# Optimization experiments

Hardware: AMD Instinct MI355X
Metric: run time of the kernel (lower is better)

## Reference

```python
import jax, jax.numpy as jnp
import numpy as np

def setup_inputs() -> dict:
    key = jax.random.key(0)
    ks = jax.random.split(key, 6)
    B, H, Dk, Dv = 128, 16, 128, 128
    return {
        "q": jax.random.normal(ks[0], (B, H, 1, Dk), dtype=jnp.float32),
        "k": jax.random.normal(ks[1], (B, H, 1, Dk), dtype=jnp.float32),
        "v": jax.random.normal(ks[2], (B, H, 1, Dv), dtype=jnp.float32),
        "g": jax.random.uniform(ks[3], (B, H, 1), dtype=jnp.float32),
        "beta": jax.random.uniform(ks[4], (B, H, 1), dtype=jnp.float32),
        "last_recurrent_state": jax.random.normal(ks[5], (B, H, Dk, Dv), dtype=jnp.float32),
    }

def reference(q, k, v, g, beta, last_recurrent_state):
    # q,k: (B,H,1,Dk); v: (B,H,1,Dv); g,beta: (B,H,1); state: (B,H,Dk,Dv)
    q_t = q[:, :, 0, :]                      # (B,H,Dk)
    k_t = k[:, :, 0, :]                      # (B,H,Dk)
    v_t = v[:, :, 0, :]                      # (B,H,Dv)
    decay = jnp.exp(g)[..., None]            # (B,H,1,1)
    state = last_recurrent_state * decay     # (B,H,Dk,Dv)
    kv_mem = jnp.einsum('bhkv,bhk->bhv', state, k_t)   # (B,H,Dv)
    delta = (v_t - kv_mem) * beta            # (B,H,Dv)
    state = state + k_t[..., :, None] * delta[..., None, :]  # outer update
    out = jnp.einsum('bhkv,bhk->bhv', state, q_t)       # (B,H,Dv)
    out = out[:, :, None, :]                 # (B,H,1,Dv)
    return jnp.concatenate([out.reshape(-1), state.reshape(-1)], axis=0)
```

## Files before the change

### kernel.cpp

```cpp
#include <hip/hip_runtime.h>


#define DK 128
#define DV 128
#define VS 32
typedef float f4 __attribute__((ext_vector_type(4)));

__global__ __launch_bounds__(256) void s1_cell_kernel(
    const float* __restrict__ q,
    const float* __restrict__ k,
    const float* __restrict__ v,
    const float* __restrict__ g,
    const float* __restrict__ beta,
    const float* __restrict__ S,
    float* __restrict__ out,
    int BH)
{
    const int bh    = blockIdx.x >> 2;
    const int sl    = blockIdx.x & 3;
    const int vbase = sl * VS;

    const size_t stile = (size_t)bh * DK * DV;
    const float* __restrict__ Sb   = S + stile + vbase;
    float* __restrict__ out_o      = out + (size_t)bh * DV + vbase;
    float* __restrict__ out_S      = out + (size_t)BH * DV + stile + vbase;

    __shared__ float kt[DK];
    __shared__ float qt[DK];
    __shared__ float vt[VS];
    __shared__ float apart[32][VS];
    __shared__ float bpart[32][VS];
    __shared__ float sdelta[VS];
    __shared__ float s_kq;

    const int t = threadIdx.x;

    if (t < DK) {
        kt[t] = k[bh * DK + t];
        qt[t] = q[bh * DK + t];
    }
    if (t < VS) vt[t] = v[bh * DV + vbase + t];
    __syncthreads();

    const float decay = expf(g[bh]);
    const float bta   = beta[bh];

    if (t < 64) {
        float val = kt[t] * qt[t] + kt[t + 64] * qt[t + 64];
        #pragma unroll
        for (int off = 32; off > 0; off >>= 1)
            val += __shfl_down(val, off, 64);
        if (t == 0) s_kq = val;
    }

    const int vc = (t & 7) * 4;
    const int rb = t >> 3;

    f4 s[4];
    float a0 = 0.f, a1 = 0.f, a2 = 0.f, a3 = 0.f;
    float b0 = 0.f, b1 = 0.f, b2 = 0.f, b3 = 0.f;

    #pragma unroll
    for (int i = 0; i < 4; ++i) {
        const int r = rb + 32 * i;
        s[i] = *(const f4*)(Sb + (size_t)r * DV + vc);
        const float kv = kt[r];
        const float qv = qt[r];
        a0 += s[i].x * kv;  a1 += s[i].y * kv;  a2 += s[i].z * kv;  a3 += s[i].w * kv;
        b0 += s[i].x * qv;  b1 += s[i].y * qv;  b2 += s[i].z * qv;  b3 += s[i].w * qv;
    }
    *(f4*)&apart[rb][vc] = (f4){a0, a1, a2, a3};
    *(f4*)&bpart[rb][vc] = (f4){b0, b1, b2, b3};
    __syncthreads();

    if (t < VS) {
        float A = 0.f, Bq = 0.f;
        #pragma unroll
        for (int j = 0; j < 32; ++j) {
            A  += apart[j][t];
            Bq += bpart[j][t];
        }
        const float dlt = (vt[t] - decay * A) * bta;
        sdelta[t] = dlt;
        __builtin_nontemporal_store(decay * Bq + s_kq * dlt, &out_o[t]);
    }
    __syncthreads();

    const f4 d = *(const f4*)&sdelta[vc];

    #pragma unroll
    for (int i = 0; i < 4; ++i) {
        const int r = rb + 32 * i;
        const float ktk = kt[r];
        f4 w;
        w.x = decay * s[i].x + ktk * d.x;
        w.y = decay * s[i].y + ktk * d.y;
        w.z = decay * s[i].z + ktk * d.z;
        w.w = decay * s[i].w + ktk * d.w;
        __builtin_nontemporal_store(w, (f4*)(out_S + (size_t)r * DV + vc));
    }
}

extern "C" void kernel_launch(void* const* d_in, const int* in_sizes, int n_in,
                              void* d_out, int out_size, void* d_ws, size_t ws_size,
                              hipStream_t stream) {
    const float* q    = (const float*)d_in[0];
    const float* k    = (const float*)d_in[1];
    const float* v    = (const float*)d_in[2];
    const float* g    = (const float*)d_in[3];
    const float* beta = (const float*)d_in[4];
    const float* S    = (const float*)d_in[5];
    float* out = (float*)d_out;

    const int BH = in_sizes[3];

    s1_cell_kernel<<<BH * 4, 256, 0, stream>>>(q, k, v, g, beta, S, out, BH);
}
```

Measured before the change: 248.7 us.

## Map each 128x32 state slice to one wavefront with shuffle reductions

Each wavefront now owns one (bh, column-slice) task, with each lane holding a 16x4 patch of the state in registers. Shared-memory staging, cross-thread partial sums and all block barriers are replaced by xor-shuffle reductions across the row groups, and k/q/v are loaded straight from global memory. This removes synchronization and LDS traffic on a memory-bound kernel. In exchange each lane keeps 16 float4 values live, which raises register pressure, and the grid has four times fewer blocks.

```diff
diff --git a/kernel.cpp b/kernel.cpp
--- a/kernel.cpp
+++ b/kernel.cpp
@@ -6,7 +6,7 @@
 #define VS 32
 typedef float f4 __attribute__((ext_vector_type(4)));
 
-__global__ __launch_bounds__(256) void s1_cell_kernel(
+__global__ __launch_bounds__(256, 4) void s1_cell_kernel(
     const float* __restrict__ q,
     const float* __restrict__ k,
     const float* __restrict__ v,
@@ -16,88 +16,74 @@
     float* __restrict__ out,
     int BH)
 {
-    const int bh    = blockIdx.x >> 2;
-    const int sl    = blockIdx.x & 3;
-    const int vbase = sl * VS;
+    const int wid  = threadIdx.x >> 6;
+    const int lane = threadIdx.x & 63;
+    const int task = (blockIdx.x << 2) + wid;
+    const int bh   = task >> 2;
+    const int sl   = task & 3;
+
+    const int vgrp = lane & 7;
+    const int kgrp = lane >> 3;
+    const int colf = sl * VS + vgrp * 4;
+    const int row0 = kgrp * 16;
 
     const size_t stile = (size_t)bh * DK * DV;
-    const float* __restrict__ Sb   = S + stile + vbase;
-    float* __restrict__ out_o      = out + (size_t)bh * DV + vbase;
-    float* __restrict__ out_S      = out + (size_t)BH * DV + stile + vbase;
-
-    __shared__ float kt[DK];
-    __shared__ float qt[DK];
-    __shared__ float vt[VS];
-    __shared__ float apart[32][VS];
-    __shared__ float bpart[32][VS];
-    __shared__ float sdelta[VS];
-    __shared__ float s_kq;
-
-    const int t = threadIdx.x;
-
-    if (t < DK) {
-        kt[t] = k[bh * DK + t];
-        qt[t] = q[bh * DK + t];
-    }
-    if (t < VS) vt[t] = v[bh * DV + vbase + t];
-    __syncthreads();
+    const float* __restrict__ Sp = S   + stile + (size_t)row0 * DV + colf;
+    float* __restrict__ So = out + (size_t)BH * DV + stile + (size_t)row0 * DV + colf;
 
     const float decay = expf(g[bh]);
     const float bta   = beta[bh];
 
-    if (t < 64) {
-        float val = kt[t] * qt[t] + kt[t + 64] * qt[t + 64];
-        #pragma unroll
-        for (int off = 32; off > 0; off >>= 1)
-            val += __shfl_down(val, off, 64);
-        if (t == 0) s_kq = val;
+    f4 kt[4];
+    #pragma unroll
+    for (int j = 0; j < 4; ++j)
+        kt[j] = *(const f4*)(k + bh * DK + row0 + 4 * j);
+
+    const f4 vv = *(const f4*)(v + bh * DV + colf);
+
+    f4 s[16];
+    #pragma unroll
+    for (int i = 0; i < 16; ++i)
+        s[i] = *(const f4*)(Sp + (size_t)i * DV);
+
+    f4 a = {0.f, 0.f, 0.f, 0.f};
+    f4 b = {0.f, 0.f, 0.f, 0.f};
+    float kq = 0.f;
+    #pragma unroll
+    for (int j = 0; j < 4; ++j) {
+        const f4 qj = *(const f4*)(q + bh * DK + row0 + 4 * j);
+        const f4 kj = kt[j];
+        a += s[4*j+0] * kj.x;  b += s[4*j+0] * qj.x;
+        a += s[4*j+1] * kj.y;  b += s[4*j+1] * qj.y;
+        a += s[4*j+2] * kj.z;  b += s[4*j+2] * qj.z;
+        a += s[4*j+3] * kj.w;  b += s[4*j+3] * qj.w;
+        kq += kj.x*qj.x + kj.y*qj.y + kj.z*qj.z + kj.w*qj.w;
     }
 
-    const int vc = (t & 7) * 4;
-    const int rb = t >> 3;
+    #pragma unroll
+    for (int m = 8; m <= 32; m <<= 1) {
+        a.x += __shfl_xor(a.x, m, 64);
+        a.y += __shfl_xor(a.y, m, 64);
+        a.z += __shfl_xor(a.z, m, 64);
+        a.w += __shfl_xor(a.w, m, 64);
+        b.x += __shfl_xor(b.x, m, 64);
+        b.y += __shfl_xor(b.y, m, 64);
+        b.z += __shfl_xor(b.z, m, 64);
+        b.w += __shfl_xor(b.w, m, 64);
+        kq  += __shfl_xor(kq,  m, 64);
+    }
 
-    f4 s[4];
-    float a0 = 0.f, a1 = 0.f, a2 = 0.f, a3 = 0.f;
-    float b0 = 0.f, b1 = 0.f, b2 = 0.f, b3 = 0.f;
+    const f4 dlt = (vv - decay * a) * bta;
+    if (kgrp == 0) {
+        const f4 o = decay * b + kq * dlt;
+        __builtin_nontemporal_store(o, (f4*)(out + (size_t)bh * DV + colf));
+    }
 
     #pragma unroll
-    for (int i = 0; i < 4; ++i) {
-        const int r = rb + 32 * i;
-        s[i] = *(const f4*)(Sb + (size_t)r * DV + vc);
-        const float kv = kt[r];
-        const float qv = qt[r];
-        a0 += s[i].x * kv;  a1 += s[i].y * kv;  a2 += s[i].z * kv;  a3 += s[i].w * kv;
-        b0 += s[i].x * qv;  b1 += s[i].y * qv;  b2 += s[i].z * qv;  b3 += s[i].w * qv;
-    }
-    *(f4*)&apart[rb][vc] = (f4){a0, a1, a2, a3};
-    *(f4*)&bpart[rb][vc] = (f4){b0, b1, b2, b3};
-    __syncthreads();
-
-    if (t < VS) {
-        float A = 0.f, Bq = 0.f;
-        #pragma unroll
-        for (int j = 0; j < 32; ++j) {
-            A  += apart[j][t];
-            Bq += bpart[j][t];
-        }
-        const float dlt = (vt[t] - decay * A) * bta;
-        sdelta[t] = dlt;
-        __builtin_nontemporal_store(decay * Bq + s_kq * dlt, &out_o[t]);
-    }
-    __syncthreads();
-
-    const f4 d = *(const f4*)&sdelta[vc];
-
-    #pragma unroll
-    for (int i = 0; i < 4; ++i) {
-        const int r = rb + 32 * i;
-        const float ktk = kt[r];
-        f4 w;
-        w.x = decay * s[i].x + ktk * d.x;
-        w.y = decay * s[i].y + ktk * d.y;
-        w.z = decay * s[i].z + ktk * d.z;
-        w.w = decay * s[i].w + ktk * d.w;
-        __builtin_nontemporal_store(w, (f4*)(out_S + (size_t)r * DV + vc));
+    for (int i = 0; i < 16; ++i) {
+        const float kv = ((const float*)kt)[i];
+        const f4 w = decay * s[i] + kv * dlt;
+        __builtin_nontemporal_store(w, (f4*)(So + (size_t)i * DV));
     }
 }
 
@@ -114,5 +100,5 @@
 
     const int BH = in_sizes[3];
 
-    s1_cell_kernel<<<BH * 4, 256, 0, stream>>>(q, k, v, g, beta, S, out, BH);
+    s1_cell_kernel<<<BH, 256, 0, stream>>>(q, k, v, g, beta, S, out, BH);
 }
```

Measured after the change: 254.1 us. +2.2%, slower.
